# Performance work log

Hardware: AMD Instinct MI355X
Metric: run time of the kernel (lower is better)

The kernel has to match this reference:

```python
import jax, jax.numpy as jnp
import numpy as np

B, N, DIM, HEADS, DEPTH, MLP = 4, 1024, 256, 4, 4, 1024
DH = DIM // HEADS
EPS = 1e-5


def _ln(x, g, b):
    mu = jnp.mean(x, axis=-1, keepdims=True)
    var = jnp.mean((x - mu) ** 2, axis=-1, keepdims=True)
    return (x - mu) / jnp.sqrt(var + EPS) * g + b


def setup_inputs() -> dict:
    key = jax.random.key(0)
    ks = jax.random.split(key, 10)
    s = 0.02
    p = {}
    p["x"] = jax.random.normal(ks[0], (B, N, DIM), jnp.float32)
    p["attn_bias"] = jax.random.normal(ks[1], (2, B, HEADS, N, N), jnp.float32)
    p["ln1_g"] = jnp.ones((DEPTH, DIM), jnp.float32)
    p["ln1_b"] = jnp.zeros((DEPTH, DIM), jnp.float32)
    p["Wkv"] = jax.random.normal(ks[2], (DEPTH, DIM, 2 * DIM), jnp.float32) * s
    p["Wq"] = jax.random.normal(ks[3], (DEPTH, DIM, DIM), jnp.float32) * s
    p["Wo"] = jax.random.normal(ks[4], (DEPTH, DIM, DIM), jnp.float32) * s
    p["bo"] = jnp.zeros((DEPTH, DIM), jnp.float32)
    p["ln2_g"] = jnp.ones((DEPTH, DIM), jnp.float32)
    p["ln2_b"] = jnp.zeros((DEPTH, DIM), jnp.float32)
    p["W1"] = jax.random.normal(ks[5], (DEPTH, DIM, MLP), jnp.float32) * s
    p["b1"] = jnp.zeros((DEPTH, MLP), jnp.float32)
    p["W2"] = jax.random.normal(ks[6], (DEPTH, MLP, DIM), jnp.float32) * s
    p["b2"] = jnp.zeros((DEPTH, DIM), jnp.float32)
    p["Wg"] = jax.random.normal(ks[7], (DIM, DIM), jnp.float32) * s
    p["lng_g"] = jnp.ones((DIM,), jnp.float32)
    p["lng_b"] = jnp.zeros((DIM,), jnp.float32)
    return p


def reference(x, attn_bias, ln1_g, ln1_b, Wkv, Wq, Wo, bo, ln2_g, ln2_b, W1, b1, W2, b2, Wg, lng_g, lng_b):
    scale = DIM ** -0.5
    add_attn = attn_bias[0] + attn_bias[1]            # [B,H,N,N]
    # aggregation bias matrices are layer-invariant (recomputed identically each layer in torch)
    A = jnp.mean(attn_bias[0], axis=1)                # [B,N,N]
    S = jnp.mean(attn_bias[1], axis=1)
    G = jax.nn.softmax(A * S, axis=2)                 # [B,N,N]

    def split_heads(t):  # [B,N,DIM] -> [B,H,N,DH]
        return t.reshape(B, N, HEADS, DH).transpose(0, 2, 1, 3)

    for l in range(DEPTH):
        # softmax-GCN aggregation
        x_ma = jax.nn.relu(_ln(jnp.matmul(G, x) @ Wg, lng_g, lng_b))
        # attention (PreNorm on x only; q comes from un-normed x_ma)
        xn = _ln(x, ln1_g[l], ln1_b[l])
        kv = xn @ Wkv[l]
        k, v = jnp.split(kv, 2, axis=-1)
        q = x_ma @ Wq[l]
        qh, kh, vh = split_heads(q), split_heads(k), split_heads(v)
        dots = jnp.einsum('bhid,bhjd->bhij', qh, kh) * scale + add_attn
        attn = jax.nn.softmax(dots, axis=-1)
        out = jnp.einsum('bhij,bhjd->bhid', attn, vh)
        out = out.transpose(0, 2, 1, 3).reshape(B, N, DIM)
        x = x + out @ Wo[l] + bo[l]
        # feed-forward (exact GELU, matching torch nn.GELU default)
        xn2 = _ln(x, ln2_g[l], ln2_b[l])
        x = x + jax.nn.gelu(xn2 @ W1[l] + b1[l], approximate=False) @ W2[l] + b2[l]
    return x
```

## Files before the change

### kernel.cpp

```cpp
#include <hip/hip_runtime.h>
#include <hip/hip_bf16.h>
#include <math.h>

typedef unsigned short u16;
typedef __bf16 bf16x8 __attribute__((ext_vector_type(8)));
typedef float f32x4 __attribute__((ext_vector_type(4)));

#define B_ 4
#define N_ 1024
#define DIM_ 256
#define HEADS_ 4
#define DH_ 64
#define MLP_ 1024
#define DEPTH_ 4

__device__ __forceinline__ float r2f(u16 r){ return __uint_as_float(((unsigned)r)<<16); }
__device__ __forceinline__ u16 f2r(float f){ __hip_bfloat16 h = __float2bfloat16(f); return *(u16*)&h; }

__device__ __forceinline__ float gelu_exact(float v){
  return 0.5f*v*(1.0f + erff(v*0.70710678118654752440f));
}

#define MFMA16(a,b,c) __builtin_amdgcn_mfma_f32_16x16x32_bf16(a,b,c,0,0,0)

__global__ void prep_bias(const float* __restrict__ bias, u16* __restrict__ G, u16* __restrict__ bsum){
  int blk = blockIdx.x;
  int i = blk & (N_-1);
  int b = blk >> 10;
  int t = threadIdx.x;
  __shared__ float red[256];
  long long base0 = ((long long)(b*HEADS_)*N_ + i)*(long long)N_;
  const long long hs = (long long)N_*N_;
  const long long cs = (long long)B_*HEADS_*N_*N_;
  int j0 = t*4;
  f32x4 a = {0.f,0.f,0.f,0.f}, s = {0.f,0.f,0.f,0.f};
  #pragma unroll
  for (int h=0;h<HEADS_;h++){
    f32x4 x0 = *(const f32x4*)(bias + base0 + h*hs + j0);
    f32x4 x1 = *(const f32x4*)(bias + cs + base0 + h*hs + j0);
    a += x0; s += x1;
    union { ushort4 u; u16 e[4]; } pk;
    #pragma unroll
    for (int k=0;k<4;k++) pk.e[k] = f2r(x0[k]+x1[k]);
    *(ushort4*)(bsum + base0 + h*hs + j0) = pk.u;
  }
  float v[4]; float lmax = -3e38f;
  #pragma unroll
  for (int k=0;k<4;k++){ v[k] = (a[k]*0.25f)*(s[k]*0.25f); lmax = fmaxf(lmax, v[k]); }
  red[t]=lmax; __syncthreads();
  for (int st=128;st>0;st>>=1){ if(t<st) red[t]=fmaxf(red[t],red[t+st]); __syncthreads(); }
  float m = red[0]; __syncthreads();
  float e[4]; float lsum = 0.f;
  #pragma unroll
  for (int k=0;k<4;k++){ e[k] = __expf(v[k]-m); lsum += e[k]; }
  red[t]=lsum; __syncthreads();
  for (int st=128;st>0;st>>=1){ if(t<st) red[t]+=red[t+st]; __syncthreads(); }
  float inv = 1.0f/red[0];
  u16* Grow = G + ((long long)b*N_ + i)*(long long)N_;
  union { ushort4 u; u16 e[4]; } pg;
  #pragma unroll
  for (int k=0;k<4;k++) pg.e[k] = f2r(e[k]*inv);
  *(ushort4*)(Grow + j0) = pg.u;
}

__global__ void ln_kernel(const float* __restrict__ X, u16* __restrict__ Y,
                          const float* __restrict__ g, const float* __restrict__ bvec){
  int row = blockIdx.x*8 + (threadIdx.x>>5);
  int cg = threadIdx.x&31;
  const float* xp = X + (long long)row*DIM_ + cg*8;
  f32x4 v0 = *(const f32x4*)xp;
  f32x4 v1 = *(const f32x4*)(xp+4);
  float s = v0[0]+v0[1]+v0[2]+v0[3]+v1[0]+v1[1]+v1[2]+v1[3];
  s += __shfl_xor(s,1); s += __shfl_xor(s,2); s += __shfl_xor(s,4); s += __shfl_xor(s,8); s += __shfl_xor(s,16);
  float mu = s*(1.0f/256.0f);
  float s2 = 0.f;
  #pragma unroll
  for (int k=0;k<4;k++){ float d=v0[k]-mu; s2 += d*d; }
  #pragma unroll
  for (int k=0;k<4;k++){ float d=v1[k]-mu; s2 += d*d; }
  s2 += __shfl_xor(s2,1); s2 += __shfl_xor(s2,2); s2 += __shfl_xor(s2,4); s2 += __shfl_xor(s2,8); s2 += __shfl_xor(s2,16);
  float rstd = rsqrtf(s2*(1.0f/256.0f)+1e-5f);
  f32x4 g0 = *(const f32x4*)(g + cg*8);
  f32x4 g1 = *(const f32x4*)(g + cg*8 + 4);
  f32x4 b0 = *(const f32x4*)(bvec + cg*8);
  f32x4 b1 = *(const f32x4*)(bvec + cg*8 + 4);
  union { ushort4 u[2]; u16 e[8]; } pk;
  #pragma unroll
  for (int k=0;k<4;k++) pk.e[k]   = f2r((v0[k]-mu)*rstd*g0[k] + b0[k]);
  #pragma unroll
  for (int k=0;k<4;k++) pk.e[4+k] = f2r((v1[k]-mu)*rstd*g1[k] + b1[k]);
  u16* yp = Y + (long long)row*DIM_ + cg*8;
  *(ushort4*)yp = pk.u[0];
  *(ushort4*)(yp+4) = pk.u[1];
}

__global__ void tcast_all(const float* __restrict__ Wkv, const float* __restrict__ Wq,
                          const float* __restrict__ Wo, const float* __restrict__ W1,
                          const float* __restrict__ W2, const float* __restrict__ Wg,
                          const float* __restrict__ xin,
                          u16* WkvT, u16* WqT, u16* WoT, u16* W1T, u16* W2T, u16* WgT, u16* xT){
  int z = blockIdx.z;
  const float* I; u16* O; int ldin, R, C;
  if (z < 4)       { I = Wkv + z*131072;      O = WkvT + z*131072;      ldin=512;  R=256;  C=512;  }
  else if (z < 8)  { I = Wq  + (z-4)*65536;   O = WqT  + (z-4)*65536;   ldin=256;  R=256;  C=256;  }
  else if (z < 12) { I = Wo  + (z-8)*65536;   O = WoT  + (z-8)*65536;   ldin=256;  R=256;  C=256;  }
  else if (z < 16) { I = W1  + (z-12)*262144; O = W1T  + (z-12)*262144; ldin=1024; R=256;  C=1024; }
  else if (z < 20) { I = W2  + (z-16)*262144; O = W2T  + (z-16)*262144; ldin=256;  R=1024; C=256;  }
  else if (z == 20){ I = Wg;                  O = WgT;                  ldin=256;  R=256;  C=256;  }
  else             { I = xin + (z-21)*262144; O = xT   + (z-21)*262144; ldin=256;  R=1024; C=256;  }
  int c0 = blockIdx.x*32, r0 = blockIdx.y*32;
  if (c0 >= C || r0 >= R) return;
  __shared__ float tile[32][33];
  int tx = threadIdx.x, ty = threadIdx.y;
  #pragma unroll
  for (int i=0;i<4;i++)
    tile[ty*4+i][tx] = I[(long long)(r0+ty*4+i)*ldin + c0+tx];
  __syncthreads();
  #pragma unroll
  for (int i=0;i<4;i++)
    O[(long long)(c0+ty*4+i)*R + r0+tx] = f2r(tile[tx][ty*4+i]);
}

__global__ __launch_bounds__(512) void layer_pre(
    const u16* __restrict__ Gb, const u16* __restrict__ xT, const u16* __restrict__ xnb,
    const u16* __restrict__ WgT, const u16* __restrict__ WqT, const u16* __restrict__ WkvT,
    const float* __restrict__ lng, const float* __restrict__ lnb,
    u16* __restrict__ qb, u16* __restrict__ kvb, u16* __restrict__ vt)
{
  __shared__ float Gx_s[16][264];
  __shared__ float t2_s[16][264];
  __shared__ u16  xma_s[16][264];
  int tid = threadIdx.x;
  int w = tid>>6, lane = tid&63, lr = lane&15, qd = lane>>4;
  int row0 = blockIdx.x*16;
  int batch = row0>>10, brow0 = row0&1023;

  {
    int kw = w>>2, cw = w&3;
    const u16* Ap = Gb + (long long)batch*1048576 + (long long)(brow0+lr)*1024 + kw*512;
    const u16* Bp = xT + (long long)batch*262144 + (long long)kw*512;
    f32x4 acc[4] = {};
    for (int k0=0;k0<512;k0+=32){
      bf16x8 af = *(const bf16x8*)(Ap + k0 + qd*8);
      #pragma unroll
      for (int nt=0;nt<4;nt++){
        bf16x8 bf = *(const bf16x8*)(Bp + (long long)(cw*64+nt*16+lr)*1024 + k0 + qd*8);
        acc[nt] = MFMA16(af,bf,acc[nt]);
      }
    }
    if (kw==0){
      #pragma unroll
      for (int nt=0;nt<4;nt++)
        #pragma unroll
        for (int r=0;r<4;r++) Gx_s[qd*4+r][cw*64+nt*16+lr] = acc[nt][r];
    }
    __syncthreads();
    if (kw==1){
      #pragma unroll
      for (int nt=0;nt<4;nt++)
        #pragma unroll
        for (int r=0;r<4;r++) Gx_s[qd*4+r][cw*64+nt*16+lr] += acc[nt][r];
    }
    __syncthreads();
  }
  {
    int r = tid>>5, cg = tid&31;
    #pragma unroll
    for (int i=0;i<8;i++) xma_s[r][cg*8+i] = f2r(Gx_s[r][cg*8+i]);
  }
  __syncthreads();
  {
    f32x4 acc[2] = {};
    for (int k0=0;k0<256;k0+=32){
      bf16x8 af = *(const bf16x8*)&xma_s[lr][k0+qd*8];
      #pragma unroll
      for (int i=0;i<2;i++){
        bf16x8 bf = *(const bf16x8*)(WgT + (long long)((w*2+i)*16+lr)*256 + k0 + qd*8);
        acc[i] = MFMA16(af,bf,acc[i]);
      }
    }
    #pragma unroll
    for (int i=0;i<2;i++)
      #pragma unroll
      for (int r=0;r<4;r++) t2_s[qd*4+r][(w*2+i)*16+lr] = acc[i][r];
  }
  __syncthreads();
  {
    int r = tid>>5, cg = tid&31;
    float v[8]; float s=0.f;
    #pragma unroll
    for (int i=0;i<8;i++){ v[i] = t2_s[r][cg*8+i]; s += v[i]; }
    s += __shfl_xor(s,1); s += __shfl_xor(s,2); s += __shfl_xor(s,4); s += __shfl_xor(s,8); s += __shfl_xor(s,16);
    float mu = s*(1.0f/256.0f);
    float s2=0.f;
    #pragma unroll
    for (int i=0;i<8;i++){ float d=v[i]-mu; s2 += d*d; }
    s2 += __shfl_xor(s2,1); s2 += __shfl_xor(s2,2); s2 += __shfl_xor(s2,4); s2 += __shfl_xor(s2,8); s2 += __shfl_xor(s2,16);
    float rstd = rsqrtf(s2*(1.0f/256.0f)+1e-5f);
    #pragma unroll
    for (int i=0;i<8;i++){
      int c = cg*8+i;
      float y = (v[i]-mu)*rstd*lng[c] + lnb[c];
      xma_s[r][c] = f2r(fmaxf(y,0.f));
    }
  }
  __syncthreads();
  {
    f32x4 acc[2] = {};
    for (int k0=0;k0<256;k0+=32){
      bf16x8 af = *(const bf16x8*)&xma_s[lr][k0+qd*8];
      #pragma unroll
      for (int i=0;i<2;i++){
        bf16x8 bf = *(const bf16x8*)(WqT + (long long)((w*2+i)*16+lr)*256 + k0 + qd*8);
        acc[i] = MFMA16(af,bf,acc[i]);
      }
    }
    #pragma unroll
    for (int i=0;i<2;i++)
      #pragma unroll
      for (int r=0;r<4;r++)
        qb[(long long)(row0+qd*4+r)*DIM_ + (w*2+i)*16+lr] = f2r(acc[i][r]);
  }
  {
    const u16* Ap = xnb + (long long)(row0+lr)*DIM_;
    f32x4 acc[4] = {};
    for (int k0=0;k0<256;k0+=32){
      bf16x8 af = *(const bf16x8*)(Ap + k0 + qd*8);
      #pragma unroll
      for (int i=0;i<4;i++){
        bf16x8 bf = *(const bf16x8*)(WkvT + (long long)((w*4+i)*16+lr)*256 + k0 + qd*8);
        acc[i] = MFMA16(af,bf,acc[i]);
      }
    }
    #pragma unroll
    for (int i=0;i<4;i++){
      int col = (w*4+i)*16+lr;
      #pragma unroll
      for (int r=0;r<4;r++){
        int row = row0+qd*4+r;
        float v = acc[i][r];
        kvb[(long long)row*512 + col] = f2r(v);
        if (col >= 256)
          vt[(long long)batch*262144 + (long long)(col-256)*1024 + (row&1023)] = f2r(v);
      }
    }
  }
}

__global__ __launch_bounds__(512) void flash_attn(
    const u16* __restrict__ qb, const u16* __restrict__ kvb,
    const u16* __restrict__ vt, const u16* __restrict__ bsum,
    u16* __restrict__ out)
{
  int z = blockIdx.z;
  int b = z>>2, h = z&3;
  int qt = blockIdx.x;
  int tid = threadIdx.x;
  int w = tid>>6, lane = tid&63;
  int g = w>>2, tw = w&3;
  int lr = lane&15, qd = lane>>4;
  __shared__ u16 Pl[8][16][72];
  __shared__ u16 sb[8][16][72];
  __shared__ float Ol[8][16][68];
  __shared__ float Ml[8][16];
  __shared__ float Ll[8][16];

  int qrow0 = qt*64 + tw*16;
  const u16* qp = qb + ((long long)(b*N_) + qrow0 + lr)*DIM_ + h*DH_;
  bf16x8 aq0 = *(const bf16x8*)(qp + qd*8);
  bf16x8 aq1 = *(const bf16x8*)(qp + 32 + qd*8);

  f32x4 oacc[4] = {};
  float m_r[4] = {-3e38f,-3e38f,-3e38f,-3e38f};
  float l_r[4] = {0.f,0.f,0.f,0.f};

  const u16* kbase = kvb + ((long long)(b*N_))*512 + h*DH_;
  const u16* vbase = vt + (long long)b*(DIM_*N_) + (long long)(h*DH_)*N_;
  const u16* bias_base = bsum + ((long long)z*N_ + qrow0)*(long long)N_;
  int srr = lane>>2, scc = (lane&3)*16;

  for (int jtl=0; jtl<8; jtl++){
    int j0 = (g*8 + jtl)*64;
    {
      const u16* gs = bias_base + (long long)srr*N_ + j0 + scc;
      uint4 t0 = *(const uint4*)gs;
      uint4 t1 = *(const uint4*)(gs+8);
      *(uint4*)&sb[w][srr][scc]   = t0;
      *(uint4*)&sb[w][srr][scc+8] = t1;
    }
    f32x4 sacc[4] = {};
    #pragma unroll
    for (int nt=0; nt<4; nt++){
      const u16* kp = kbase + (long long)(j0 + nt*16 + lr)*512;
      bf16x8 bk0 = *(const bf16x8*)(kp + qd*8);
      bf16x8 bk1 = *(const bf16x8*)(kp + 32 + qd*8);
      sacc[nt] = MFMA16(aq0, bk0, sacc[nt]);
      sacc[nt] = MFMA16(aq1, bk1, sacc[nt]);
    }
    #pragma unroll
    for (int r=0;r<4;r++){
      float pv[4];
      float vmax = -3e38f;
      #pragma unroll
      for (int nt=0;nt<4;nt++){
        float v = sacc[nt][r]*0.0625f + r2f(sb[w][qd*4+r][nt*16+lr]);
        pv[nt] = v;
        vmax = fmaxf(vmax, v);
      }
      vmax = fmaxf(vmax, __shfl_xor(vmax,1));
      vmax = fmaxf(vmax, __shfl_xor(vmax,2));
      vmax = fmaxf(vmax, __shfl_xor(vmax,4));
      vmax = fmaxf(vmax, __shfl_xor(vmax,8));
      float newm = fmaxf(m_r[r], vmax);
      float alpha = __expf(m_r[r]-newm);
      m_r[r] = newm;
      float psum = 0.f;
      #pragma unroll
      for (int nt=0;nt<4;nt++){
        float p = __expf(pv[nt]-newm);
        psum += p;
        Pl[w][qd*4+r][nt*16+lr] = f2r(p);
      }
      psum += __shfl_xor(psum,1);
      psum += __shfl_xor(psum,2);
      psum += __shfl_xor(psum,4);
      psum += __shfl_xor(psum,8);
      l_r[r] = l_r[r]*alpha + psum;
      #pragma unroll
      for (int ot=0;ot<4;ot++) oacc[ot][r] *= alpha;
    }
    #pragma unroll
    for (int ks=0;ks<2;ks++){
      bf16x8 ap = *(const bf16x8*)&Pl[w][lr][ks*32 + qd*8];
      #pragma unroll
      for (int ot=0;ot<4;ot++){
        const u16* vp = vbase + (long long)(ot*16+lr)*N_ + j0 + ks*32 + qd*8;
        bf16x8 bv = *(const bf16x8*)vp;
        oacc[ot] = MFMA16(ap, bv, oacc[ot]);
      }
    }
  }
  #pragma unroll
  for (int r=0;r<4;r++){
    int row = qd*4+r;
    #pragma unroll
    for (int ot=0;ot<4;ot++) Ol[w][row][ot*16+lr] = oacc[ot][r];
    if (lr==0){ Ml[w][row] = m_r[r]; Ll[w][row] = l_r[r]; }
  }
  __syncthreads();
  if (w < 4){
    #pragma unroll
    for (int r=0;r<4;r++){
      int row = qd*4+r;
      float m0 = Ml[w][row], m1 = Ml[w+4][row];
      float mm = fmaxf(m0,m1);
      float e0 = __expf(m0-mm), e1 = __expf(m1-mm);
      float inv = 1.0f/(Ll[w][row]*e0 + Ll[w+4][row]*e1);
      #pragma unroll
      for (int ot=0;ot<4;ot++){
        float o = Ol[w][row][ot*16+lr]*e0 + Ol[w+4][row][ot*16+lr]*e1;
        out[((long long)(b*N_) + qrow0 + row)*DIM_ + h*DH_ + ot*16 + lr] = f2r(o*inv);
      }
    }
  }
}

__global__ __launch_bounds__(512) void layer_post(
    const u16* __restrict__ aob, const float* __restrict__ resx,
    const u16* __restrict__ WoT, const float* __restrict__ bo,
    const float* __restrict__ ln2g, const float* __restrict__ ln2b,
    const u16* __restrict__ W1T, const float* __restrict__ b1,
    const u16* __restrict__ W2T, const float* __restrict__ b2,
    float* __restrict__ xf_out,
    const float* __restrict__ ln1g_next, const float* __restrict__ ln1b_next,
    u16* __restrict__ xn_out, u16* __restrict__ xT_out)
{
  __shared__ float v_s[16][264];
  __shared__ u16  xn2_s[16][264];
  __shared__ u16  h1_s[16][1048];
  __shared__ float xnew_s[16][264];
  int tid = threadIdx.x;
  int w = tid>>6, lane = tid&63, lr = lane&15, qd = lane>>4;
  int row0 = blockIdx.x*16;
  int batch = row0>>10;

  {
    const u16* Ap = aob + (long long)(row0+lr)*DIM_;
    f32x4 acc[2] = {};
    for (int k0=0;k0<256;k0+=32){
      bf16x8 af = *(const bf16x8*)(Ap + k0 + qd*8);
      #pragma unroll
      for (int i=0;i<2;i++){
        bf16x8 bf = *(const bf16x8*)(WoT + (long long)((w*2+i)*16+lr)*256 + k0 + qd*8);
        acc[i] = MFMA16(af,bf,acc[i]);
      }
    }
    #pragma unroll
    for (int i=0;i<2;i++){
      int col = (w*2+i)*16+lr;
      #pragma unroll
      for (int r=0;r<4;r++)
        v_s[qd*4+r][col] = acc[i][r] + bo[col] + resx[(long long)(row0+qd*4+r)*DIM_ + col];
    }
  }
  __syncthreads();
  {
    int r = tid>>5, cg = tid&31;
    float v[8]; float s=0.f;
    #pragma unroll
    for (int i=0;i<8;i++){ v[i] = v_s[r][cg*8+i]; s += v[i]; }
    s += __shfl_xor(s,1); s += __shfl_xor(s,2); s += __shfl_xor(s,4); s += __shfl_xor(s,8); s += __shfl_xor(s,16);
    float mu = s*(1.0f/256.0f);
    float s2=0.f;
    #pragma unroll
    for (int i=0;i<8;i++){ float d=v[i]-mu; s2 += d*d; }
    s2 += __shfl_xor(s2,1); s2 += __shfl_xor(s2,2); s2 += __shfl_xor(s2,4); s2 += __shfl_xor(s2,8); s2 += __shfl_xor(s2,16);
    float rstd = rsqrtf(s2*(1.0f/256.0f)+1e-5f);
    #pragma unroll
    for (int i=0;i<8;i++){
      int c = cg*8+i;
      xn2_s[r][c] = f2r((v[i]-mu)*rstd*ln2g[c] + ln2b[c]);
    }
  }
  __syncthreads();
  {
    f32x4 acc[8] = {};
    for (int k0=0;k0<256;k0+=32){
      bf16x8 af = *(const bf16x8*)&xn2_s[lr][k0+qd*8];
      #pragma unroll
      for (int i=0;i<8;i++){
        bf16x8 bf = *(const bf16x8*)(W1T + (long long)((w*8+i)*16+lr)*256 + k0 + qd*8);
        acc[i] = MFMA16(af,bf,acc[i]);
      }
    }
    #pragma unroll
    for (int i=0;i<8;i++){
      int col = (w*8+i)*16+lr;
      #pragma unroll
      for (int r=0;r<4;r++)
        h1_s[qd*4+r][col] = f2r(gelu_exact(acc[i][r] + b1[col]));
    }
  }
  __syncthreads();
  {
    f32x4 acc[2] = {};
    for (int k0=0;k0<1024;k0+=32){
      bf16x8 af = *(const bf16x8*)&h1_s[lr][k0+qd*8];
      #pragma unroll
      for (int i=0;i<2;i++){
        bf16x8 bf = *(const bf16x8*)(W2T + (long long)((w*2+i)*16+lr)*1024 + k0 + qd*8);
        acc[i] = MFMA16(af,bf,acc[i]);
      }
    }
    #pragma unroll
    for (int i=0;i<2;i++){
      int col = (w*2+i)*16+lr;
      #pragma unroll
      for (int r=0;r<4;r++){
        float v = acc[i][r] + b2[col] + v_s[qd*4+r][col];
        xf_out[(long long)(row0+qd*4+r)*DIM_ + col] = v;
        xnew_s[qd*4+r][col] = v;
      }
    }
  }
  if (ln1g_next){
    __syncthreads();
    int r = tid>>5, cg = tid&31;
    float v[8]; float s=0.f;
    #pragma unroll
    for (int i=0;i<8;i++){ v[i] = xnew_s[r][cg*8+i]; s += v[i]; }
    s += __shfl_xor(s,1); s += __shfl_xor(s,2); s += __shfl_xor(s,4); s += __shfl_xor(s,8); s += __shfl_xor(s,16);
    float mu = s*(1.0f/256.0f);
    float s2=0.f;
    #pragma unroll
    for (int i=0;i<8;i++){ float d=v[i]-mu; s2 += d*d; }
    s2 += __shfl_xor(s2,1); s2 += __shfl_xor(s2,2); s2 += __shfl_xor(s2,4); s2 += __shfl_xor(s2,8); s2 += __shfl_xor(s2,16);
    float rstd = rsqrtf(s2*(1.0f/256.0f)+1e-5f);
    int grow = row0 + r;
    #pragma unroll
    for (int i=0;i<8;i++){
      int c = cg*8+i;
      xn_out[(long long)grow*DIM_ + c] = f2r((v[i]-mu)*rstd*ln1g_next[c] + ln1b_next[c]);
      xT_out[(long long)batch*262144 + (long long)c*1024 + (grow&1023)] = f2r(v[i]);
    }
  }
}

extern "C" void kernel_launch(void* const* d_in, const int* in_sizes, int n_in,
                              void* d_out, int out_size, void* d_ws, size_t ws_size,
                              hipStream_t stream){
  const float* x_in   = (const float*)d_in[0];
  const float* abias  = (const float*)d_in[1];
  const float* ln1_g  = (const float*)d_in[2];
  const float* ln1_b  = (const float*)d_in[3];
  const float* Wkv    = (const float*)d_in[4];
  const float* Wq     = (const float*)d_in[5];
  const float* Wo     = (const float*)d_in[6];
  const float* bo     = (const float*)d_in[7];
  const float* ln2_g  = (const float*)d_in[8];
  const float* ln2_b  = (const float*)d_in[9];
  const float* W1     = (const float*)d_in[10];
  const float* b1     = (const float*)d_in[11];
  const float* W2     = (const float*)d_in[12];
  const float* b2     = (const float*)d_in[13];
  const float* Wg     = (const float*)d_in[14];
  const float* lng_g  = (const float*)d_in[15];
  const float* lng_b  = (const float*)d_in[16];

  char* ws = (char*)d_ws;
  float* xf   = (float*)(ws);
  u16*  Gb    = (u16*)(ws + (4ll<<20));
  u16*  bsum  = (u16*)(ws + (12ll<<20));
  u16*  kvb   = (u16*)(ws + (44ll<<20));
  u16*  vt    = (u16*)(ws + (48ll<<20));
  u16*  xT    = (u16*)(ws + (50ll<<20));
  u16*  xnb   = (u16*)(ws + (52ll<<20));
  u16*  qb    = (u16*)(ws + (54ll<<20));
  u16*  aob   = (u16*)(ws + (56ll<<20));
  u16*  WkvT  = (u16*)(ws + (58ll<<20));
  u16*  WqT   = (u16*)(ws + (59ll<<20));
  u16*  WoT   = (u16*)(ws + (59ll<<20) + (512ll<<10));
  u16*  W1T   = (u16*)(ws + (60ll<<20));
  u16*  W2T   = (u16*)(ws + (62ll<<20));
  u16*  WgT   = (u16*)(ws + (64ll<<20));

  dim3 b256(256), b512(512);

  prep_bias<<<dim3(B_*N_), b256, 0, stream>>>(abias, Gb, bsum);
  tcast_all<<<dim3(32,32,25), dim3(32,8), 0, stream>>>(Wkv,Wq,Wo,W1,W2,Wg,x_in,
                                                       WkvT,WqT,WoT,W1T,W2T,WgT,xT);
  ln_kernel<<<dim3(512), b256, 0, stream>>>(x_in, xnb, ln1_g, ln1_b);

  for (int l=0; l<DEPTH_; l++){
    const float* resx = (l==0) ? x_in : xf;
    layer_pre<<<dim3(256), b512, 0, stream>>>(Gb, xT, xnb,
        WgT, WqT + (long long)l*65536, WkvT + (long long)l*131072,
        lng_g, lng_b, qb, kvb, vt);
    flash_attn<<<dim3(16,1,B_*HEADS_), b512, 0, stream>>>(qb, kvb, vt, bsum, aob);
    if (l < DEPTH_-1){
      layer_post<<<dim3(256), b512, 0, stream>>>(aob, resx,
          WoT + (long long)l*65536, bo + l*DIM_, ln2_g + l*DIM_, ln2_b + l*DIM_,
          W1T + (long long)l*262144, b1 + l*MLP_, W2T + (long long)l*262144, b2 + l*DIM_,
          xf, ln1_g + (l+1)*DIM_, ln1_b + (l+1)*DIM_, xnb, xT);
    } else {
      layer_post<<<dim3(256), b512, 0, stream>>>(aob, resx,
          WoT + (long long)l*65536, bo + l*DIM_, ln2_g + l*DIM_, ln2_b + l*DIM_,
          W1T + (long long)l*262144, b1 + l*MLP_, W2T + (long long)l*262144, b2 + l*DIM_,
          (float*)d_out, nullptr, nullptr, nullptr, nullptr);
    }
  }
}
```

Measured before the change: 760.9 us.

## Fuse per-layer kernels into one cooperative persistent kernel with grid syncs

Replaces the twelve per-layer launches (pre, flash attention, post for each of four layers) with a single cooperative kernel of 256 blocks. It runs the three stages in sequence with grid-wide barriers and reuses one shared-memory buffer across stages. The goal is to remove launch gaps and per-kernel ramp-up and tail costs between dependent stages. In exchange, every block waits at each grid barrier. The launch bound of two blocks per CU with about 74 KB of shared memory each may also limit register allocation.

```diff
diff --git a/kernel.cpp b/kernel.cpp
--- a/kernel.cpp
+++ b/kernel.cpp
@@ -1,6 +1,9 @@
 #include <hip/hip_runtime.h>
+#include <hip/hip_cooperative_groups.h>
 #include <hip/hip_bf16.h>
 #include <math.h>
+
+namespace cg = cooperative_groups;
 
 typedef unsigned short u16;
 typedef __bf16 bf16x8 __attribute__((ext_vector_type(8)));
@@ -121,24 +124,36 @@
     O[(long long)(c0+ty*4+i)*R + r0+tx] = f2r(tile[tx][ty*4+i]);
 }
 
-__global__ __launch_bounds__(512) void layer_pre(
-    const u16* __restrict__ Gb, const u16* __restrict__ xT, const u16* __restrict__ xnb,
-    const u16* __restrict__ WgT, const u16* __restrict__ WqT, const u16* __restrict__ WkvT,
-    const float* __restrict__ lng, const float* __restrict__ lnb,
-    u16* __restrict__ qb, u16* __restrict__ kvb, u16* __restrict__ vt)
-{
-  __shared__ float Gx_s[16][264];
-  __shared__ float t2_s[16][264];
-  __shared__ u16  xma_s[16][264];
-  int tid = threadIdx.x;
+struct MegaArgs {
+  const u16* Gb; const u16* bsum;
+  u16* xT; u16* xnb;
+  const u16* WgT; const u16* WqT; const u16* WkvT;
+  const u16* WoT; const u16* W1T; const u16* W2T;
+  const float* lng_g; const float* lng_b;
+  const float* ln1_g; const float* ln1_b;
+  const float* ln2_g; const float* ln2_b;
+  const float* bo; const float* b1; const float* b2;
+  const float* x_in; float* xf; float* out_f;
+  u16* qb; u16* kvb; u16* vt; u16* aob;
+};
+
+#define SMEM_BYTES 75776
+
+__device__ __forceinline__ void pre_stage(const MegaArgs& A, int l, char* smem, int tid, int bid){
+  float (*Gx_s)[264] = (float(*)[264])smem;
+  float (*t2_s)[264] = (float(*)[264])(smem+16896);
+  u16  (*xma_s)[264] = (u16 (*)[264])(smem+33792);
+  const u16* WqTl  = A.WqT  + (long long)l*65536;
+  const u16* WkvTl = A.WkvT + (long long)l*131072;
+
   int w = tid>>6, lane = tid&63, lr = lane&15, qd = lane>>4;
-  int row0 = blockIdx.x*16;
+  int row0 = bid*16;
   int batch = row0>>10, brow0 = row0&1023;
 
   {
     int kw = w>>2, cw = w&3;
-    const u16* Ap = Gb + (long long)batch*1048576 + (long long)(brow0+lr)*1024 + kw*512;
-    const u16* Bp = xT + (long long)batch*262144 + (long long)kw*512;
+    const u16* Ap = A.Gb + (long long)batch*1048576 + (long long)(brow0+lr)*1024 + kw*512;
+    const u16* Bp = A.xT + (long long)batch*262144 + (long long)kw*512;
     f32x4 acc[4] = {};
     for (int k0=0;k0<512;k0+=32){
       bf16x8 af = *(const bf16x8*)(Ap + k0 + qd*8);
@@ -164,9 +179,9 @@
     __syncthreads();
   }
   {
-    int r = tid>>5, cg = tid&31;
-    #pragma unroll
-    for (int i=0;i<8;i++) xma_s[r][cg*8+i] = f2r(Gx_s[r][cg*8+i]);
+    int r = tid>>5, cg2 = tid&31;
+    #pragma unroll
+    for (int i=0;i<8;i++) xma_s[r][cg2*8+i] = f2r(Gx_s[r][cg2*8+i]);
   }
   __syncthreads();
   {
@@ -175,7 +190,7 @@
       bf16x8 af = *(const bf16x8*)&xma_s[lr][k0+qd*8];
       #pragma unroll
       for (int i=0;i<2;i++){
-        bf16x8 bf = *(const bf16x8*)(WgT + (long long)((w*2+i)*16+lr)*256 + k0 + qd*8);
+        bf16x8 bf = *(const bf16x8*)(A.WgT + (long long)((w*2+i)*16+lr)*256 + k0 + qd*8);
         acc[i] = MFMA16(af,bf,acc[i]);
       }
     }
@@ -186,10 +201,10 @@
   }
   __syncthreads();
   {
-    int r = tid>>5, cg = tid&31;
+    int r = tid>>5, cg2 = tid&31;
     float v[8]; float s=0.f;
     #pragma unroll
-    for (int i=0;i<8;i++){ v[i] = t2_s[r][cg*8+i]; s += v[i]; }
+    for (int i=0;i<8;i++){ v[i] = t2_s[r][cg2*8+i]; s += v[i]; }
     s += __shfl_xor(s,1); s += __shfl_xor(s,2); s += __shfl_xor(s,4); s += __shfl_xor(s,8); s += __shfl_xor(s,16);
     float mu = s*(1.0f/256.0f);
     float s2=0.f;
@@ -199,8 +214,8 @@
     float rstd = rsqrtf(s2*(1.0f/256.0f)+1e-5f);
     #pragma unroll
     for (int i=0;i<8;i++){
-      int c = cg*8+i;
-      float y = (v[i]-mu)*rstd*lng[c] + lnb[c];
+      int c = cg2*8+i;
+      float y = (v[i]-mu)*rstd*A.lng_g[c] + A.lng_b[c];
       xma_s[r][c] = f2r(fmaxf(y,0.f));
     }
   }
@@ -211,7 +226,7 @@
       bf16x8 af = *(const bf16x8*)&xma_s[lr][k0+qd*8];
       #pragma unroll
       for (int i=0;i<2;i++){
-        bf16x8 bf = *(const bf16x8*)(WqT + (long long)((w*2+i)*16+lr)*256 + k0 + qd*8);
+        bf16x8 bf = *(const bf16x8*)(WqTl + (long long)((w*2+i)*16+lr)*256 + k0 + qd*8);
         acc[i] = MFMA16(af,bf,acc[i]);
       }
     }
@@ -219,16 +234,16 @@
     for (int i=0;i<2;i++)
       #pragma unroll
       for (int r=0;r<4;r++)
-        qb[(long long)(row0+qd*4+r)*DIM_ + (w*2+i)*16+lr] = f2r(acc[i][r]);
-  }
-  {
-    const u16* Ap = xnb + (long long)(row0+lr)*DIM_;
+        A.qb[(long long)(row0+qd*4+r)*DIM_ + (w*2+i)*16+lr] = f2r(acc[i][r]);
+  }
+  {
+    const u16* Ap = A.xnb + (long long)(row0+lr)*DIM_;
     f32x4 acc[4] = {};
     for (int k0=0;k0<256;k0+=32){
       bf16x8 af = *(const bf16x8*)(Ap + k0 + qd*8);
       #pragma unroll
       for (int i=0;i<4;i++){
-        bf16x8 bf = *(const bf16x8*)(WkvT + (long long)((w*4+i)*16+lr)*256 + k0 + qd*8);
+        bf16x8 bf = *(const bf16x8*)(WkvTl + (long long)((w*4+i)*16+lr)*256 + k0 + qd*8);
         acc[i] = MFMA16(af,bf,acc[i]);
       }
     }
@@ -239,34 +254,30 @@
       for (int r=0;r<4;r++){
         int row = row0+qd*4+r;
         float v = acc[i][r];
-        kvb[(long long)row*512 + col] = f2r(v);
+        A.kvb[(long long)row*512 + col] = f2r(v);
         if (col >= 256)
-          vt[(long long)batch*262144 + (long long)(col-256)*1024 + (row&1023)] = f2r(v);
-      }
-    }
-  }
-}
-
-__global__ __launch_bounds__(512) void flash_attn(
-    const u16* __restrict__ qb, const u16* __restrict__ kvb,
-    const u16* __restrict__ vt, const u16* __restrict__ bsum,
-    u16* __restrict__ out)
-{
-  int z = blockIdx.z;
+          A.vt[(long long)batch*262144 + (long long)(col-256)*1024 + (row&1023)] = f2r(v);
+      }
+    }
+  }
+}
+
+__device__ __forceinline__ void flash_stage(const MegaArgs& A, char* smem, int tid, int bid){
+  u16 (*Pl)[16][72]  = (u16 (*)[16][72])smem;
+  u16 (*sb)[16][72]  = (u16 (*)[16][72])(smem+18432);
+  float (*Ol)[16][68]= (float(*)[16][68])(smem+36864);
+  float (*Ml)[16]    = (float(*)[16])(smem+71680);
+  float (*Ll)[16]    = (float(*)[16])(smem+72192);
+
+  int qt = bid & 15;
+  int z  = bid >> 4;
   int b = z>>2, h = z&3;
-  int qt = blockIdx.x;
-  int tid = threadIdx.x;
   int w = tid>>6, lane = tid&63;
   int g = w>>2, tw = w&3;
   int lr = lane&15, qd = lane>>4;
-  __shared__ u16 Pl[8][16][72];
-  __shared__ u16 sb[8][16][72];
-  __shared__ float Ol[8][16][68];
-  __shared__ float Ml[8][16];
-  __shared__ float Ll[8][16];
 
   int qrow0 = qt*64 + tw*16;
-  const u16* qp = qb + ((long long)(b*N_) + qrow0 + lr)*DIM_ + h*DH_;
+  const u16* qp = A.qb + ((long long)(b*N_) + qrow0 + lr)*DIM_ + h*DH_;
   bf16x8 aq0 = *(const bf16x8*)(qp + qd*8);
   bf16x8 aq1 = *(const bf16x8*)(qp + 32 + qd*8);
 
@@ -274,9 +285,9 @@
   float m_r[4] = {-3e38f,-3e38f,-3e38f,-3e38f};
   float l_r[4] = {0.f,0.f,0.f,0.f};
 
-  const u16* kbase = kvb + ((long long)(b*N_))*512 + h*DH_;
-  const u16* vbase = vt + (long long)b*(DIM_*N_) + (long long)(h*DH_)*N_;
-  const u16* bias_base = bsum + ((long long)z*N_ + qrow0)*(long long)N_;
+  const u16* kbase = A.kvb + ((long long)(b*N_))*512 + h*DH_;
+  const u16* vbase = A.vt + (long long)b*(DIM_*N_) + (long long)(h*DH_)*N_;
+  const u16* bias_base = A.bsum + ((long long)z*N_ + qrow0)*(long long)N_;
   int srr = lane>>2, scc = (lane&3)*16;
 
   for (int jtl=0; jtl<8; jtl++){
@@ -359,39 +370,44 @@
       #pragma unroll
       for (int ot=0;ot<4;ot++){
         float o = Ol[w][row][ot*16+lr]*e0 + Ol[w+4][row][ot*16+lr]*e1;
-        out[((long long)(b*N_) + qrow0 + row)*DIM_ + h*DH_ + ot*16 + lr] = f2r(o*inv);
-      }
-    }
-  }
-}
-
-__global__ __launch_bounds__(512) void layer_post(
-    const u16* __restrict__ aob, const float* __restrict__ resx,
-    const u16* __restrict__ WoT, const float* __restrict__ bo,
-    const float* __restrict__ ln2g, const float* __restrict__ ln2b,
-    const u16* __restrict__ W1T, const float* __restrict__ b1,
-    const u16* __restrict__ W2T, const float* __restrict__ b2,
-    float* __restrict__ xf_out,
-    const float* __restrict__ ln1g_next, const float* __restrict__ ln1b_next,
-    u16* __restrict__ xn_out, u16* __restrict__ xT_out)
-{
-  __shared__ float v_s[16][264];
-  __shared__ u16  xn2_s[16][264];
-  __shared__ u16  h1_s[16][1048];
-  __shared__ float xnew_s[16][264];
-  int tid = threadIdx.x;
+        A.aob[((long long)(b*N_) + qrow0 + row)*DIM_ + h*DH_ + ot*16 + lr] = f2r(o*inv);
+      }
+    }
+  }
+}
+
+__device__ __forceinline__ void post_stage(const MegaArgs& A, int l, char* smem, int tid, int bid){
+  float (*v_s)[264]   = (float(*)[264])smem;
+  u16  (*xn2_s)[264]  = (u16 (*)[264])(smem+16896);
+  u16  (*h1_s)[1048]  = (u16 (*)[1048])(smem+25344);
+  float (*xnew_s)[264]= (float(*)[264])(smem+58880);
+
+  const float* resx = (l==0) ? A.x_in : A.xf;
+  float* xout = (l==DEPTH_-1) ? A.out_f : A.xf;
+  const u16* WoTl = A.WoT + (long long)l*65536;
+  const u16* W1Tl = A.W1T + (long long)l*262144;
+  const u16* W2Tl = A.W2T + (long long)l*262144;
+  const float* bol   = A.bo   + l*DIM_;
+  const float* ln2gl = A.ln2_g + l*DIM_;
+  const float* ln2bl = A.ln2_b + l*DIM_;
+  const float* b1l   = A.b1   + l*MLP_;
+  const float* b2l   = A.b2   + l*DIM_;
+  bool has_next = (l < DEPTH_-1);
+  const float* ln1g_n = A.ln1_g + (l+1)*DIM_;
+  const float* ln1b_n = A.ln1_b + (l+1)*DIM_;
+
   int w = tid>>6, lane = tid&63, lr = lane&15, qd = lane>>4;
-  int row0 = blockIdx.x*16;
+  int row0 = bid*16;
   int batch = row0>>10;
 
   {
-    const u16* Ap = aob + (long long)(row0+lr)*DIM_;
+    const u16* Ap = A.aob + (long long)(row0+lr)*DIM_;
     f32x4 acc[2] = {};
     for (int k0=0;k0<256;k0+=32){
       bf16x8 af = *(const bf16x8*)(Ap + k0 + qd*8);
       #pragma unroll
       for (int i=0;i<2;i++){
-        bf16x8 bf = *(const bf16x8*)(WoT + (long long)((w*2+i)*16+lr)*256 + k0 + qd*8);
+        bf16x8 bf = *(const bf16x8*)(WoTl + (long long)((w*2+i)*16+lr)*256 + k0 + qd*8);
         acc[i] = MFMA16(af,bf,acc[i]);
       }
     }
@@ -400,15 +416,15 @@
       int col = (w*2+i)*16+lr;
       #pragma unroll
       for (int r=0;r<4;r++)
-        v_s[qd*4+r][col] = acc[i][r] + bo[col] + resx[(long long)(row0+qd*4+r)*DIM_ + col];
-    }
-  }
-  __syncthreads();
-  {
-    int r = tid>>5, cg = tid&31;
+        v_s[qd*4+r][col] = acc[i][r] + bol[col] + resx[(long long)(row0+qd*4+r)*DIM_ + col];
+    }
+  }
+  __syncthreads();
+  {
+    int r = tid>>5, cg2 = tid&31;
     float v[8]; float s=0.f;
     #pragma unroll
-    for (int i=0;i<8;i++){ v[i] = v_s[r][cg*8+i]; s += v[i]; }
+    for (int i=0;i<8;i++){ v[i] = v_s[r][cg2*8+i]; s += v[i]; }
     s += __shfl_xor(s,1); s += __shfl_xor(s,2); s += __shfl_xor(s,4); s += __shfl_xor(s,8); s += __shfl_xor(s,16);
     float mu = s*(1.0f/256.0f);
     float s2=0.f;
@@ -418,8 +434,8 @@
     float rstd = rsqrtf(s2*(1.0f/256.0f)+1e-5f);
     #pragma unroll
     for (int i=0;i<8;i++){
-      int c = cg*8+i;
-      xn2_s[r][c] = f2r((v[i]-mu)*rstd*ln2g[c] + ln2b[c]);
+      int c = cg2*8+i;
+      xn2_s[r][c] = f2r((v[i]-mu)*rstd*ln2gl[c] + ln2bl[c]);
     }
   }
   __syncthreads();
@@ -429,7 +445,7 @@
       bf16x8 af = *(const bf16x8*)&xn2_s[lr][k0+qd*8];
       #pragma unroll
       for (int i=0;i<8;i++){
-        bf16x8 bf = *(const bf16x8*)(W1T + (long long)((w*8+i)*16+lr)*256 + k0 + qd*8);
+        bf16x8 bf = *(const bf16x8*)(W1Tl + (long long)((w*8+i)*16+lr)*256 + k0 + qd*8);
         acc[i] = MFMA16(af,bf,acc[i]);
       }
     }
@@ -438,7 +454,7 @@
       int col = (w*8+i)*16+lr;
       #pragma unroll
       for (int r=0;r<4;r++)
-        h1_s[qd*4+r][col] = f2r(gelu_exact(acc[i][r] + b1[col]));
+        h1_s[qd*4+r][col] = f2r(gelu_exact(acc[i][r] + b1l[col]));
     }
   }
   __syncthreads();
@@ -448,7 +464,7 @@
       bf16x8 af = *(const bf16x8*)&h1_s[lr][k0+qd*8];
       #pragma unroll
       for (int i=0;i<2;i++){
-        bf16x8 bf = *(const bf16x8*)(W2T + (long long)((w*2+i)*16+lr)*1024 + k0 + qd*8);
+        bf16x8 bf = *(const bf16x8*)(W2Tl + (long long)((w*2+i)*16+lr)*1024 + k0 + qd*8);
         acc[i] = MFMA16(af,bf,acc[i]);
       }
     }
@@ -457,18 +473,18 @@
       int col = (w*2+i)*16+lr;
       #pragma unroll
       for (int r=0;r<4;r++){
-        float v = acc[i][r] + b2[col] + v_s[qd*4+r][col];
-        xf_out[(long long)(row0+qd*4+r)*DIM_ + col] = v;
+        float v = acc[i][r] + b2l[col] + v_s[qd*4+r][col];
+        xout[(long long)(row0+qd*4+r)*DIM_ + col] = v;
         xnew_s[qd*4+r][col] = v;
       }
     }
   }
-  if (ln1g_next){
+  if (has_next){
     __syncthreads();
-    int r = tid>>5, cg = tid&31;
+    int r = tid>>5, cg2 = tid&31;
     float v[8]; float s=0.f;
     #pragma unroll
-    for (int i=0;i<8;i++){ v[i] = xnew_s[r][cg*8+i]; s += v[i]; }
+    for (int i=0;i<8;i++){ v[i] = xnew_s[r][cg2*8+i]; s += v[i]; }
     s += __shfl_xor(s,1); s += __shfl_xor(s,2); s += __shfl_xor(s,4); s += __shfl_xor(s,8); s += __shfl_xor(s,16);
     float mu = s*(1.0f/256.0f);
     float s2=0.f;
@@ -479,10 +495,24 @@
     int grow = row0 + r;
     #pragma unroll
     for (int i=0;i<8;i++){
-      int c = cg*8+i;
-      xn_out[(long long)grow*DIM_ + c] = f2r((v[i]-mu)*rstd*ln1g_next[c] + ln1b_next[c]);
-      xT_out[(long long)batch*262144 + (long long)c*1024 + (grow&1023)] = f2r(v[i]);
-    }
+      int c = cg2*8+i;
+      A.xnb[(long long)grow*DIM_ + c] = f2r((v[i]-mu)*rstd*ln1g_n[c] + ln1b_n[c]);
+      A.xT[(long long)batch*262144 + (long long)c*1024 + (grow&1023)] = f2r(v[i]);
+    }
+  }
+}
+
+__global__ __launch_bounds__(512, 2) void mega_kernel(MegaArgs A){
+  cg::grid_group grid = cg::this_grid();
+  __shared__ __align__(16) char smem[SMEM_BYTES];
+  int tid = threadIdx.x, bid = blockIdx.x;
+  for (int l=0; l<DEPTH_; l++){
+    pre_stage(A, l, smem, tid, bid);
+    grid.sync();
+    flash_stage(A, smem, tid, bid);
+    grid.sync();
+    post_stage(A, l, smem, tid, bid);
+    if (l < DEPTH_-1) grid.sync();
   }
 }
 
@@ -524,29 +554,22 @@
   u16*  W2T   = (u16*)(ws + (62ll<<20));
   u16*  WgT   = (u16*)(ws + (64ll<<20));
 
-  dim3 b256(256), b512(512);
-
-  prep_bias<<<dim3(B_*N_), b256, 0, stream>>>(abias, Gb, bsum);
+  prep_bias<<<dim3(B_*N_), dim3(256), 0, stream>>>(abias, Gb, bsum);
   tcast_all<<<dim3(32,32,25), dim3(32,8), 0, stream>>>(Wkv,Wq,Wo,W1,W2,Wg,x_in,
                                                        WkvT,WqT,WoT,W1T,W2T,WgT,xT);
-  ln_kernel<<<dim3(512), b256, 0, stream>>>(x_in, xnb, ln1_g, ln1_b);
-
-  for (int l=0; l<DEPTH_; l++){
-    const float* resx = (l==0) ? x_in : xf;
-    layer_pre<<<dim3(256), b512, 0, stream>>>(Gb, xT, xnb,
-        WgT, WqT + (long long)l*65536, WkvT + (long long)l*131072,
-        lng_g, lng_b, qb, kvb, vt);
-    flash_attn<<<dim3(16,1,B_*HEADS_), b512, 0, stream>>>(qb, kvb, vt, bsum, aob);
-    if (l < DEPTH_-1){
-      layer_post<<<dim3(256), b512, 0, stream>>>(aob, resx,
-          WoT + (long long)l*65536, bo + l*DIM_, ln2_g + l*DIM_, ln2_b + l*DIM_,
-          W1T + (long long)l*262144, b1 + l*MLP_, W2T + (long long)l*262144, b2 + l*DIM_,
-          xf, ln1_g + (l+1)*DIM_, ln1_b + (l+1)*DIM_, xnb, xT);
-    } else {
-      layer_post<<<dim3(256), b512, 0, stream>>>(aob, resx,
-          WoT + (long long)l*65536, bo + l*DIM_, ln2_g + l*DIM_, ln2_b + l*DIM_,
-          W1T + (long long)l*262144, b1 + l*MLP_, W2T + (long long)l*262144, b2 + l*DIM_,
-          (float*)d_out, nullptr, nullptr, nullptr, nullptr);
-    }
-  }
-}
+  ln_kernel<<<dim3(512), dim3(256), 0, stream>>>(x_in, xnb, ln1_g, ln1_b);
+
+  MegaArgs a;
+  a.Gb = Gb; a.bsum = bsum; a.xT = xT; a.xnb = xnb;
+  a.WgT = WgT; a.WqT = WqT; a.WkvT = WkvT;
+  a.WoT = WoT; a.W1T = W1T; a.W2T = W2T;
+  a.lng_g = lng_g; a.lng_b = lng_b;
+  a.ln1_g = ln1_g; a.ln1_b = ln1_b;
+  a.ln2_g = ln2_g; a.ln2_b = ln2_b;
+  a.bo = bo; a.b1 = b1; a.b2 = b2;
+  a.x_in = x_in; a.xf = xf; a.out_f = (float*)d_out;
+  a.qb = qb; a.kvb = kvb; a.vt = vt; a.aob = aob;
+
+  void* kargs[] = { (void*)&a };
+  hipLaunchCooperativeKernel((void*)mega_kernel, dim3(256), dim3(512), kargs, 0, stream);
+}
```

New measurement: 1.205 ms. 58.4% more time.
